# Performance work log

Hardware: AMD Instinct MI355X
Metric: run time of the kernel (lower is better)

## Reference

```python
import jax, jax.numpy as jnp
import numpy as np

MAX_DIM = 2 ** 14  # hard-coded in the original module
DIM = 512


def setup_inputs() -> dict:
    key = jax.random.key(0)
    emb = jax.random.normal(key, (MAX_DIM, DIM), dtype=jnp.float32)
    return {
        "embedding": emb,
        "batch_size": 16,
        "n_obs_support": 8192,
        "n_obs_query": 4096,
    }


def reference(embedding, batch_size, n_obs_support, n_obs_query):
    # torch.multinomial with uniform weights and replacement=False is
    # equivalent to taking the first k elements of a uniform random
    # permutation of [0, MAX_DIM) per batch row. We realize that with a
    # parallel random-key top-k: draw iid uniforms, take top-(n_s+n_q)
    # indices -> k distinct uniformly-distributed indices per row.
    n_total = n_obs_support + n_obs_query
    assert n_total <= MAX_DIM, "Number of observations is too large."
    key = jax.random.key(42)
    scores = jax.random.uniform(key, (batch_size, MAX_DIM), dtype=jnp.float32)
    _, indices = jax.lax.top_k(scores, n_total)  # (B, n_total), distinct per row
    x = embedding[indices]                       # (B, n_total, DIM) gather
    x_support = x[:, :n_obs_support]
    x_query = x[:, n_obs_support:n_total]
    return (x_support, x_query)
```

## Files before the change

kernel.cpp:

```cpp
#include <hip/hip_runtime.h>
#include <stdint.h>

#define NBATCH 16
#define NOBS   16384
#define NSUP   8192
#define NQRY   4096
#define NTOT   12288
#define DIMV   128
#define NBINS  4096
#define BINSHIFT 11

typedef float f32x4 __attribute__((ext_vector_type(4)));

__device__ __forceinline__ uint32_t rotl32(uint32_t x, int r) {
  return (x << r) | (x >> (32 - r));
}

__device__ __forceinline__ void threefry2x32_k42(uint32_t& x0, uint32_t& x1) {
  const uint32_t ks0 = 0u;
  const uint32_t ks1 = 42u;
  const uint32_t ks2 = 0u ^ 42u ^ 0x1BD11BDAu;
  x0 += ks0; x1 += ks1;
#define TF_ROUND(r) { x0 += x1; x1 = rotl32(x1, (r)); x1 ^= x0; }
  TF_ROUND(13) TF_ROUND(15) TF_ROUND(26) TF_ROUND(6)
  x0 += ks1; x1 += ks2 + 1u;
  TF_ROUND(17) TF_ROUND(29) TF_ROUND(16) TF_ROUND(24)
  x0 += ks2; x1 += ks0 + 2u;
  TF_ROUND(13) TF_ROUND(15) TF_ROUND(26) TF_ROUND(6)
  x0 += ks0; x1 += ks1 + 3u;
  TF_ROUND(17) TF_ROUND(29) TF_ROUND(16) TF_ROUND(24)
  x0 += ks1; x1 += ks2 + 4u;
  TF_ROUND(13) TF_ROUND(15) TF_ROUND(26) TF_ROUND(6)
  x0 += ks2; x1 += ks0 + 5u;
#undef TF_ROUND
}

__device__ __forceinline__ uint32_t jax_key(uint32_t f) {
  uint32_t x0 = 0u, x1 = f;
  threefry2x32_k42(x0, x1);
  return (x0 ^ x1) >> 9;
}

__device__ __forceinline__ uint32_t pack_cmp(uint32_t key, uint32_t idx_in_row) {
  return ((key & 0x7FFu) << 14) | (16383u - idx_in_row);
}

__global__ void __launch_bounds__(1024)
k_rank16(uint16_t* __restrict__ rmat) {
  __shared__ uint32_t bucket[NOBS];
  __shared__ uint32_t hist[NBINS];
  __shared__ uint32_t base[NBINS];
  __shared__ uint32_t cursor[NBINS];
  __shared__ uint32_t wtot[16];
  __shared__ uint32_t wafter[16];

  const int b    = blockIdx.x;
  const int tid  = threadIdx.x;
  const int wid  = tid >> 6;
  const int lane = tid & 63;

#pragma unroll
  for (int k = 0; k < 4; ++k) hist[tid * 4 + k] = 0u;
  __syncthreads();

  uint32_t key[16];
#pragma unroll
  for (int i = 0; i < 16; ++i) {
    key[i] = jax_key((uint32_t)(b * NOBS + i * 1024 + tid));
    atomicAdd(&hist[key[i] >> BINSHIFT], 1u);
  }
  __syncthreads();

  const uint32_t c0 = hist[tid * 4 + 0];
  const uint32_t c1 = hist[tid * 4 + 1];
  const uint32_t c2 = hist[tid * 4 + 2];
  const uint32_t c3 = hist[tid * 4 + 3];
  const uint32_t s  = c0 + c1 + c2 + c3;
  uint32_t v = s;
#pragma unroll
  for (int off = 1; off < 64; off <<= 1) {
    const uint32_t nb = __shfl_down(v, off);
    v += (lane + off < 64) ? nb : 0u;
  }
  if (lane == 0) wtot[wid] = v;
  __syncthreads();
  if (wid == 0) {
    const uint32_t t = (lane < 16) ? wtot[lane] : 0u;
    uint32_t u = t;
#pragma unroll
    for (int off = 1; off < 16; off <<= 1) {
      const uint32_t nb = __shfl_down(u, off);
      u += (lane + off < 64) ? nb : 0u;
    }
    if (lane < 16) wafter[lane] = u - t;
  }
  __syncthreads();
  const uint32_t after = (v - s) + wafter[wid];
  base[tid * 4 + 3] = after;
  base[tid * 4 + 2] = after + c3;
  base[tid * 4 + 1] = after + c3 + c2;
  base[tid * 4 + 0] = after + c3 + c2 + c1;
  cursor[tid * 4 + 3] = after;
  cursor[tid * 4 + 2] = after + c3;
  cursor[tid * 4 + 1] = after + c3 + c2;
  cursor[tid * 4 + 0] = after + c3 + c2 + c1;
  __syncthreads();

  uint32_t me[16];
#pragma unroll
  for (int i = 0; i < 16; ++i) {
    me[i] = pack_cmp(key[i], (uint32_t)(i * 1024 + tid));
    const uint32_t pos = atomicAdd(&cursor[key[i] >> BINSHIFT], 1u);
    bucket[pos] = me[i];
  }
  __syncthreads();

#pragma unroll 1
  for (int i = 0; i < 16; ++i) {
    const uint32_t bin = key[i] >> BINSHIFT;
    const uint32_t lob = base[bin];
    const uint32_t n   = hist[bin];
    uint32_t cnt = 0;
    for (uint32_t q = 0; q < n; ++q) cnt += (bucket[lob + q] > me[i]) ? 1u : 0u;
    rmat[(size_t)(i * 1024 + tid) * NBATCH + b] = (uint16_t)(lob + cnt);
  }
}

__global__ void __launch_bounds__(256)
k_gather(const uint16_t* __restrict__ rmat,
         const f32x4* __restrict__ emb,
         f32x4* __restrict__ out) {
  __shared__ uint32_t srank[NBATCH];
  const uint32_t idx = blockIdx.x;
  const int tid  = threadIdx.x;
  const int w    = tid >> 6;
  const int lane = tid & 63;

  const f32x4* s = emb + (size_t)idx * DIMV;
  const f32x4 v0 = s[lane];
  const f32x4 v1 = s[lane + 64];

  if (tid < NBATCH) srank[tid] = rmat[(size_t)idx * NBATCH + tid];
  __syncthreads();

#pragma unroll
  for (int j = 0; j < 4; ++j) {
    const int b = w * 4 + j;
    const uint32_t r = srank[b];
    if (r < NTOT) {
      size_t dofs;
      if (r < NSUP) dofs = ((size_t)b * NSUP + r) * DIMV;
      else          dofs = (size_t)NBATCH * NSUP * DIMV
                         + ((size_t)b * NQRY + (size_t)(r - NSUP)) * DIMV;
      f32x4* d = out + dofs;
      d[lane]      = v0;
      d[lane + 64] = v1;
    }
  }
}

extern "C" void kernel_launch(void* const* d_in, const int* in_sizes, int n_in,
                              void* d_out, int out_size, void* d_ws, size_t ws_size,
                              hipStream_t stream) {
  const float* emb = (const float*)d_in[0];
  uint16_t* rmat = (uint16_t*)d_ws;

  k_rank16<<<NBATCH, 1024, 0, stream>>>(rmat);
  k_gather<<<NOBS, 256, 0, stream>>>(rmat, (const f32x4*)emb, (f32x4*)d_out);
}
```

Before: 110.6 us.

## Move per-element rank counting from 16-block prep kernel into the gather kernel

```diff
diff --git a/kernel.cpp b/kernel.cpp
--- a/kernel.cpp
+++ b/kernel.cpp
@@ -46,10 +46,9 @@
 }
 
 __global__ void __launch_bounds__(1024)
-k_rank16(uint16_t* __restrict__ rmat) {
+k_prep(uint32_t* __restrict__ meta_g, uint32_t* __restrict__ bucket_g) {
   __shared__ uint32_t bucket[NOBS];
   __shared__ uint32_t hist[NBINS];
-  __shared__ uint32_t base[NBINS];
   __shared__ uint32_t cursor[NBINS];
   __shared__ uint32_t wtot[16];
   __shared__ uint32_t wafter[16];
@@ -96,38 +95,36 @@
   }
   __syncthreads();
   const uint32_t after = (v - s) + wafter[wid];
-  base[tid * 4 + 3] = after;
-  base[tid * 4 + 2] = after + c3;
-  base[tid * 4 + 1] = after + c3 + c2;
-  base[tid * 4 + 0] = after + c3 + c2 + c1;
-  cursor[tid * 4 + 3] = after;
-  cursor[tid * 4 + 2] = after + c3;
-  cursor[tid * 4 + 1] = after + c3 + c2;
-  cursor[tid * 4 + 0] = after + c3 + c2 + c1;
+  const uint32_t b3 = after;
+  const uint32_t b2 = after + c3;
+  const uint32_t b1 = after + c3 + c2;
+  const uint32_t b0 = after + c3 + c2 + c1;
+  cursor[tid * 4 + 0] = b0;
+  cursor[tid * 4 + 1] = b1;
+  cursor[tid * 4 + 2] = b2;
+  cursor[tid * 4 + 3] = b3;
+  uint32_t* mo = meta_g + (size_t)b * NBINS + tid * 4;
+  mo[0] = (b0 << 16) | c0;
+  mo[1] = (b1 << 16) | c1;
+  mo[2] = (b2 << 16) | c2;
+  mo[3] = (b3 << 16) | c3;
   __syncthreads();
 
-  uint32_t me[16];
 #pragma unroll
   for (int i = 0; i < 16; ++i) {
-    me[i] = pack_cmp(key[i], (uint32_t)(i * 1024 + tid));
+    const uint32_t me  = pack_cmp(key[i], (uint32_t)(i * 1024 + tid));
     const uint32_t pos = atomicAdd(&cursor[key[i] >> BINSHIFT], 1u);
-    bucket[pos] = me[i];
+    bucket[pos] = me;
   }
   __syncthreads();
-
-#pragma unroll 1
-  for (int i = 0; i < 16; ++i) {
-    const uint32_t bin = key[i] >> BINSHIFT;
-    const uint32_t lob = base[bin];
-    const uint32_t n   = hist[bin];
-    uint32_t cnt = 0;
-    for (uint32_t q = 0; q < n; ++q) cnt += (bucket[lob + q] > me[i]) ? 1u : 0u;
-    rmat[(size_t)(i * 1024 + tid) * NBATCH + b] = (uint16_t)(lob + cnt);
-  }
+  uint32_t* bo = bucket_g + (size_t)b * NOBS;
+#pragma unroll
+  for (int i = 0; i < 16; ++i) bo[i * 1024 + tid] = bucket[i * 1024 + tid];
 }
 
 __global__ void __launch_bounds__(256)
-k_gather(const uint16_t* __restrict__ rmat,
+k_gather(const uint32_t* __restrict__ meta_g,
+         const uint32_t* __restrict__ bucket_g,
          const f32x4* __restrict__ emb,
          f32x4* __restrict__ out) {
   __shared__ uint32_t srank[NBATCH];
@@ -140,7 +137,19 @@
   const f32x4 v0 = s[lane];
   const f32x4 v1 = s[lane + 64];
 
-  if (tid < NBATCH) srank[tid] = rmat[(size_t)idx * NBATCH + tid];
+  if (tid < NBATCH) {
+    const uint32_t b    = (uint32_t)tid;
+    const uint32_t key  = jax_key(b * NOBS + idx);
+    const uint32_t bin  = key >> BINSHIFT;
+    const uint32_t meta = meta_g[b * NBINS + bin];
+    const uint32_t lob  = meta >> 16;
+    const uint32_t n    = meta & 0xFFFFu;
+    const uint32_t me   = pack_cmp(key, idx);
+    const uint32_t* bk  = bucket_g + b * NOBS + lob;
+    uint32_t cnt = 0;
+    for (uint32_t q = 0; q < n; ++q) cnt += (bk[q] > me) ? 1u : 0u;
+    srank[b] = lob + cnt;
+  }
   __syncthreads();
 
 #pragma unroll
@@ -163,8 +172,11 @@
                               void* d_out, int out_size, void* d_ws, size_t ws_size,
                               hipStream_t stream) {
   const float* emb = (const float*)d_in[0];
-  uint16_t* rmat = (uint16_t*)d_ws;
 
-  k_rank16<<<NBATCH, 1024, 0, stream>>>(rmat);
-  k_gather<<<NOBS, 256, 0, stream>>>(rmat, (const f32x4*)emb, (f32x4*)d_out);
+  uint32_t* meta   = (uint32_t*)d_ws;
+  uint32_t* bucket = meta + NBATCH * NBINS;
+
+  k_prep  <<<NBATCH, 1024, 0, stream>>>(meta, bucket);
+  k_gather<<<NOBS, 256, 0, stream>>>(meta, bucket, (const f32x4*)emb,
+                                     (f32x4*)d_out);
 }
```

Result: no change. 108.8 us (-1.6%).
